# Kernel tuning notes

Measured on AMD Instinct MI355X. Metric: run time of the kernel, lower is better.

The kernel has to match this reference:

```python
import jax, jax.numpy as jnp
import numpy as np

B, T, IN, H0, H1, OUT = 128, 1024, 64, 256, 256, 64


def setup_inputs() -> dict:
    key = jax.random.key(0)
    ks = jax.random.split(key, 12)
    s0 = 1.0 / np.sqrt(H0)
    s1 = 1.0 / np.sqrt(H1)
    u = lambda k, shape, s: jax.random.uniform(k, shape, jnp.float32, -s, s)
    return {
        "input": jax.random.normal(ks[0], (B, T, IN), jnp.float32),
        # PyTorch LSTMCell params: weight_ih [4H, in], weight_hh [4H, H], biases [4H]
        "W_ih0": u(ks[1], (4 * H0, IN), s0),
        "W_hh0": u(ks[2], (4 * H0, H0), s0),
        "b_ih0": u(ks[3], (4 * H0,), s0),
        "b_hh0": u(ks[4], (4 * H0,), s0),
        "W_ih1": u(ks[5], (4 * H1, H0), s1),
        "W_hh1": u(ks[6], (4 * H1, H1), s1),
        "b_ih1": u(ks[7], (4 * H1,), s1),
        "b_hh1": u(ks[8], (4 * H1,), s1),
        "W_lin": u(ks[9], (OUT, H1), s1),
        "b_lin": u(ks[10], (OUT,), s1),
    }


def _lstm_cell(x_t, h, c, W_ih, W_hh, b):
    # gates in PyTorch order: i, f, g, o
    gates = x_t @ W_ih.T + h @ W_hh.T + b  # [B, 4H]
    i, f, g, o = jnp.split(gates, 4, axis=-1)
    c_new = jax.nn.sigmoid(f) * c + jax.nn.sigmoid(i) * jnp.tanh(g)
    h_new = jax.nn.sigmoid(o) * jnp.tanh(c_new)
    return h_new, c_new


def reference(input, W_ih0, W_hh0, b_ih0, b_hh0, W_ih1, W_hh1, b_ih1, b_hh1, W_lin, b_lin):
    b0 = b_ih0 + b_hh0
    b1 = b_ih1 + b_hh1
    batch = input.shape[0]
    h0 = jnp.zeros((batch, H0), input.dtype)
    c0 = jnp.zeros((batch, H0), input.dtype)
    h1 = jnp.zeros((batch, H1), input.dtype)
    c1 = jnp.zeros((batch, H1), input.dtype)

    def step(carry, x_t):
        h0, c0, h1, c1 = carry
        h0, c0 = _lstm_cell(x_t, h0, c0, W_ih0, W_hh0, b0)
        h1, c1 = _lstm_cell(h0, h1, c1, W_ih1, W_hh1, b1)
        out = h1 @ W_lin.T + b_lin  # [B, OUT]
        return (h0, c0, h1, c1), out

    xs = jnp.swapaxes(input, 0, 1)  # [T, B, IN]
    _, ys = jax.lax.scan(step, (h0, c0, h1, c1), xs)
    return jnp.swapaxes(ys, 0, 1)  # [B, T, OUT]
```

## Files before the change

kernel.cpp:

```cpp
#include <hip/hip_runtime.h>
#include <math.h>

#define TSEQ 1024
#define NB   128
#define NIN  64
#define NH   256
#define NOUT 64
#define NWG  256
#define NTHR 512
#define HS   (NH * NB)

__global__ void xpose_kernel(const float* __restrict__ in, float* __restrict__ xT) {
  __shared__ float tile[64 * 129];
  const int t = blockIdx.x;
  {
    const int b  = threadIdx.x >> 1;
    const int k0 = (threadIdx.x & 1) * 32;
    const float* src = in + (size_t)b * (TSEQ * NIN) + (size_t)t * NIN + k0;
#pragma unroll 8
    for (int k = 0; k < 32; ++k) tile[(k0 + k) * 129 + b] = src[k];
  }
  __syncthreads();
  {
    const int k  = threadIdx.x >> 2;
    const int b0 = (threadIdx.x & 3) * 32;
    float* dst = xT + (size_t)t * (NIN * NB) + (size_t)k * NB + b0;
#pragma unroll 8
    for (int i = 0; i < 32; ++i) dst[i] = tile[k * 129 + b0 + i];
  }
}

__device__ __forceinline__ float sigm(float v) { return 1.0f / (1.0f + expf(-v)); }

#define DPP_ADD(a, ctrl) do {                                                   \
  int _t = __builtin_amdgcn_update_dpp(0, __float_as_int(a), ctrl, 0xf, 0xf, true); \
  (a) += __int_as_float(_t); } while (0)

#define FMA32(w4, v0, v1) do {                                            \
  _Pragma("unroll")                                                        \
  for (int g = 0; g < 4; ++g) {                                            \
    float wg = (g == 0) ? (w4).x : (g == 1) ? (w4).y : (g == 2) ? (w4).z : (w4).w; \
    acc[g][0] += wg * (v0).x; acc[g][1] += wg * (v0).y;                    \
    acc[g][2] += wg * (v0).z; acc[g][3] += wg * (v0).w;                    \
    acc[g][4] += wg * (v1).x; acc[g][5] += wg * (v1).y;                    \
    acc[g][6] += wg * (v1).z; acc[g][7] += wg * (v1).w;                    \
  } } while (0)

__global__ __launch_bounds__(NTHR, 1) void lstm_persist(
    const float* __restrict__ x,
    const float* __restrict__ Wih0, const float* __restrict__ Whh0,
    const float* __restrict__ bih0, const float* __restrict__ bhh0,
    const float* __restrict__ Wih1, const float* __restrict__ Whh1,
    const float* __restrict__ bih1, const float* __restrict__ bhh1,
    const float* __restrict__ Wlin, const float* __restrict__ blin,
    float* __restrict__ out,
    float* __restrict__ h0T, float* __restrict__ h1T,
    const float* __restrict__ xT, unsigned* __restrict__ flags, int use_xT)
{
  __shared__ float Wt0[320 * 32];
  __shared__ float Wt1[512 * 32];
  __shared__ float Wlin2[2 * 256];
  __shared__ float red[8 * 580];
  __shared__ float redO[288];
  __shared__ float bias0[32], bias1[32], blinS[2];
  __shared__ float c0l[128], c1l[128];
  __shared__ float hs0[256 * 16];
  __shared__ float hs1[256 * 16];

  const int tid  = threadIdx.x;
  const int a    = blockIdx.x & 7;
  const int j    = blockIdx.x >> 3;
  const int b0   = a * 16;
  const int jh0  = j * 8;
  const int lane = tid & 63;
  const int wv   = tid >> 6;
  const int bh   = wv & 1;
  const int kw4  = wv >> 1;
  const int cl   = lane >> 3;
  const int kp   = lane & 7;
  const int kq   = kw4 * 8 + kp;

  for (int idx = tid; idx < 32 * 320; idx += NTHR) {
    int row = idx / 320, k = idx % 320;
    int c = row >> 2, g = row & 3;
    int grow = g * 256 + jh0 + c;
    float v = (k < 64) ? Wih0[grow * 64 + k] : Whh0[grow * 256 + (k - 64)];
    Wt0[k * 32 + row] = v;
  }
  for (int idx = tid; idx < 32 * 512; idx += NTHR) {
    int row = idx >> 9, k = idx & 511;
    int c = row >> 2, g = row & 3;
    int grow = g * 256 + jh0 + c;
    float v = (k < 256) ? Wih1[grow * 256 + k] : Whh1[grow * 256 + (k - 256)];
    Wt1[k * 32 + row] = v;
  }
  if (tid < 512) {
    int o2 = tid >> 8, k = tid & 255;
    Wlin2[tid] = Wlin[(2 * j + o2) * 256 + k];
  }
  if (tid < 32) {
    int c = tid >> 2, g = tid & 3;
    int grow = g * 256 + jh0 + c;
    bias0[tid] = bih0[grow] + bhh0[grow];
    bias1[tid] = bih1[grow] + bhh1[grow];
  }
  if (tid < 2) blinS[tid] = blin[2 * j + tid];
  if (tid < 128) { c0l[tid] = 0.0f; c1l[tid] = 0.0f; }
  __syncthreads();

  const int myflag = (a * 32 + j) * 16;

  for (int it = 0; it <= TSEQ + 1; ++it) {
    if (it >= 1 && tid < 64) {
      const unsigned tgt = (unsigned)it;
      const int fi = (a * 32 + (tid & 31)) * 16;
      while (true) {
        unsigned v = __hip_atomic_load(&flags[fi], __ATOMIC_RELAXED, __HIP_MEMORY_SCOPE_AGENT);
        if (__ballot(v >= tgt) == ~0ull) break;
        __builtin_amdgcn_s_sleep(1);
      }
    }
    __syncthreads();

    const float* h0r = h0T + ((it + 1) & 1) * HS;
    float*       h0w = h0T + (it & 1) * HS;
    const float* h1r = h1T + ((it + 1) % 3) * HS;
    float*       h1w = h1T + ((it + 2) % 3) * HS;

#pragma unroll
    for (int q = 0; q < 4; ++q) {
      int f = q * 512 + tid;
      int k = f >> 3, bi = f & 7;
      unsigned long long v0 = __hip_atomic_load(
          (const unsigned long long*)(h0r + (size_t)k * NB + b0) + bi,
          __ATOMIC_RELAXED, __HIP_MEMORY_SCOPE_AGENT);
      unsigned long long v1 = __hip_atomic_load(
          (const unsigned long long*)(h1r + (size_t)k * NB + b0) + bi,
          __ATOMIC_RELAXED, __HIP_MEMORY_SCOPE_AGENT);
      *(unsigned long long*)&hs0[f * 2] = v0;
      *(unsigned long long*)&hs1[f * 2] = v1;
    }
    __syncthreads();

    if (it < TSEQ) {
      float acc[4][8];
#pragma unroll
      for (int g = 0; g < 4; ++g)
#pragma unroll
        for (int b = 0; b < 8; ++b) acc[g][b] = 0.0f;
      if (use_xT) {
#pragma unroll
        for (int j2 = 0; j2 < 2; ++j2) {
          int k = j2 * 32 + kq;
          float4 w4 = *(const float4*)&Wt0[k * 32 + cl * 4];
          const float* xp = xT + (size_t)it * (NIN * NB) + (size_t)k * NB + b0 + bh * 8;
          float4 v0 = *(const float4*)xp;
          float4 v1 = *(const float4*)(xp + 4);
          FMA32(w4, v0, v1);
        }
      } else {
#pragma unroll
        for (int j2 = 0; j2 < 2; ++j2) {
          int k = j2 * 32 + kq;
          float4 w4 = *(const float4*)&Wt0[k * 32 + cl * 4];
          float xv[8];
#pragma unroll
          for (int b = 0; b < 8; ++b)
            xv[b] = x[(size_t)(b0 + bh * 8 + b) * (TSEQ * NIN) + (size_t)it * NIN + k];
          float4 v0 = make_float4(xv[0], xv[1], xv[2], xv[3]);
          float4 v1 = make_float4(xv[4], xv[5], xv[6], xv[7]);
          FMA32(w4, v0, v1);
        }
      }
#pragma unroll 4
      for (int j2 = 2; j2 < 10; ++j2) {
        int k = j2 * 32 + kq;
        float4 w4 = *(const float4*)&Wt0[k * 32 + cl * 4];
        const float* hp = &hs0[(k - 64) * 16 + bh * 8];
        float4 v0 = *(const float4*)hp;
        float4 v1 = *(const float4*)(hp + 4);
        FMA32(w4, v0, v1);
      }
#pragma unroll
      for (int g = 0; g < 4; ++g)
#pragma unroll
        for (int b = 0; b < 8; ++b) {
          DPP_ADD(acc[g][b], 0x104);
          DPP_ADD(acc[g][b], 0x102);
          DPP_ADD(acc[g][b], 0x101);
        }
      if (kp == 0) {
        int sbase = kw4 * 580 + (cl * 4) * 18 + bh * 8;
#pragma unroll
        for (int g = 0; g < 4; ++g)
#pragma unroll
          for (int b2 = 0; b2 < 4; ++b2)
            *(float2*)&red[sbase + g * 18 + 2 * b2] =
                make_float2(acc[g][2 * b2], acc[g][2 * b2 + 1]);
      }
    }
    if (it >= 1 && it <= TSEQ) {
      float acc[4][8];
#pragma unroll
      for (int g = 0; g < 4; ++g)
#pragma unroll
        for (int b = 0; b < 8; ++b) acc[g][b] = 0.0f;
#pragma unroll 4
      for (int j2 = 0; j2 < 8; ++j2) {
        int k = j2 * 32 + kq;
        float4 w4 = *(const float4*)&Wt1[k * 32 + cl * 4];
        const float* hp = &hs0[k * 16 + bh * 8];
        float4 v0 = *(const float4*)hp;
        float4 v1 = *(const float4*)(hp + 4);
        FMA32(w4, v0, v1);
      }
#pragma unroll 4
      for (int j2 = 8; j2 < 16; ++j2) {
        int k = j2 * 32 + kq;
        float4 w4 = *(const float4*)&Wt1[k * 32 + cl * 4];
        const float* hp = &hs1[(k - 256) * 16 + bh * 8];
        float4 v0 = *(const float4*)hp;
        float4 v1 = *(const float4*)(hp + 4);
        FMA32(w4, v0, v1);
      }
#pragma unroll
      for (int g = 0; g < 4; ++g)
#pragma unroll
        for (int b = 0; b < 8; ++b) {
          DPP_ADD(acc[g][b], 0x104);
          DPP_ADD(acc[g][b], 0x102);
          DPP_ADD(acc[g][b], 0x101);
        }
      if (kp == 0) {
        int sbase = (4 + kw4) * 580 + (cl * 4) * 18 + bh * 8;
#pragma unroll
        for (int g = 0; g < 4; ++g)
#pragma unroll
          for (int b2 = 0; b2 < 4; ++b2)
            *(float2*)&red[sbase + g * 18 + 2 * b2] =
                make_float2(acc[g][2 * b2], acc[g][2 * b2 + 1]);
      }
    }
    __syncthreads();

    if (tid < 128) {
      if (it < TSEQ) {
        int c = tid >> 4, b = tid & 15;
        float s0 = bias0[c * 4 + 0], s1 = bias0[c * 4 + 1];
        float s2 = bias0[c * 4 + 2], s3 = bias0[c * 4 + 3];
#pragma unroll
        for (int s = 0; s < 4; ++s) {
          int base = s * 580 + (c * 4) * 18 + b;
          s0 += red[base];      s1 += red[base + 18];
          s2 += red[base + 36]; s3 += red[base + 54];
        }
        float ig = sigm(s0), fg = sigm(s1), gg = tanhf(s2), og = sigm(s3);
        float cn = fg * c0l[tid] + ig * gg;
        c0l[tid] = cn;
        __hip_atomic_store(&h0w[(jh0 + c) * NB + b0 + b], og * tanhf(cn),
                           __ATOMIC_RELAXED, __HIP_MEMORY_SCOPE_AGENT);
      }
    } else if (tid < 256) {
      if (it >= 1 && it <= TSEQ) {
        int idx = tid - 128;
        int c = idx >> 4, b = idx & 15;
        float s0 = bias1[c * 4 + 0], s1 = bias1[c * 4 + 1];
        float s2 = bias1[c * 4 + 2], s3 = bias1[c * 4 + 3];
#pragma unroll
        for (int s = 4; s < 8; ++s) {
          int base = s * 580 + (c * 4) * 18 + b;
          s0 += red[base];      s1 += red[base + 18];
          s2 += red[base + 36]; s3 += red[base + 54];
        }
        float ig = sigm(s0), fg = sigm(s1), gg = tanhf(s2), og = sigm(s3);
        float cn = fg * c1l[idx] + ig * gg;
        c1l[idx] = cn;
        __hip_atomic_store(&h1w[(jh0 + c) * NB + b0 + b], og * tanhf(cn),
                           __ATOMIC_RELAXED, __HIP_MEMORY_SCOPE_AGENT);
      }
    } else {
      if (it >= 2) {
        int idx = tid & 255;
        int o2 = idx & 1, b = (idx >> 1) & 15, ks = idx >> 5;
        float acc = 0.0f;
#pragma unroll 8
        for (int k = 32 * ks; k < 32 * ks + 32; ++k)
          acc += Wlin2[o2 * 256 + k] * hs1[k * 16 + b];
        redO[(o2 * 16 + b) * 9 + ks] = acc;
      }
    }
    __syncthreads();

    if (it <= TSEQ && tid == 0) {
      asm volatile("" ::: "memory");
      __hip_atomic_store(&flags[myflag], (unsigned)(it + 1),
                         __ATOMIC_RELAXED, __HIP_MEMORY_SCOPE_AGENT);
    }

    if (it >= 2 && tid < 32) {
      int o2 = tid & 1, b = tid >> 1;
      float s = blinS[o2];
#pragma unroll
      for (int q = 0; q < 8; ++q) s += redO[(o2 * 16 + b) * 9 + q];
      out[(size_t)(b0 + b) * (TSEQ * NOUT) + (size_t)(it - 2) * NOUT + (2 * j + o2)] = s;
    }
  }
}

extern "C" void kernel_launch(void* const* d_in, const int* in_sizes, int n_in,
                              void* d_out, int out_size, void* d_ws, size_t ws_size,
                              hipStream_t stream) {
  const float* x    = (const float*)d_in[0];
  const float* Wih0 = (const float*)d_in[1];
  const float* Whh0 = (const float*)d_in[2];
  const float* bih0 = (const float*)d_in[3];
  const float* bhh0 = (const float*)d_in[4];
  const float* Wih1 = (const float*)d_in[5];
  const float* Whh1 = (const float*)d_in[6];
  const float* bih1 = (const float*)d_in[7];
  const float* bhh1 = (const float*)d_in[8];
  const float* Wlin = (const float*)d_in[9];
  const float* blin = (const float*)d_in[10];
  float* out = (float*)d_out;

  char* ws = (char*)d_ws;
  unsigned* flags = (unsigned*)ws;
  float* h0T = (float*)(ws + 16384);
  float* h1T = (float*)(ws + 16384 + 262144);
  float* xT  = (float*)(ws + (1 << 20));

  const size_t need_xT = (size_t)(1 << 20) + (size_t)TSEQ * NIN * NB * sizeof(float);
  const int use_xT = (ws_size >= need_xT) ? 1 : 0;

  size_t zbytes = (ws_size < (size_t)(1 << 20)) ? ws_size : (size_t)(1 << 20);
  hipMemsetAsync(d_ws, 0, zbytes, stream);

  if (use_xT) xpose_kernel<<<TSEQ, 256, 0, stream>>>(x, xT);

  lstm_persist<<<NWG, NTHR, 0, stream>>>(
      x, Wih0, Whh0, bih0, bhh0, Wih1, Whh1, bih1, bhh1, Wlin, blin,
      out, h0T, h1T, xT, flags, use_xT);
}
```

Baseline: 8.015 ms.

## Overlap x loads and output projection with flag wait; swizzle hidden staging

Moves the x-input load and the output-linear partial sums ahead of the inter-workgroup flag spin, so they overlap with the grid-wide wait. The output stage is delayed one more step and its computation is spread across all 512 threads. The layer-0 input FMAs now run between the global h loads and the shared-memory stores, hiding load latency. It also XOR-swizzles the hs0/hs1 layout to avoid LDS bank conflicts and keeps cell state in registers. In exchange the pipeline gets one extra iteration, an extra flag round, and more register pressure.

```diff
diff --git a/kernel.cpp b/kernel.cpp
--- a/kernel.cpp
+++ b/kernel.cpp
@@ -61,9 +61,8 @@
   __shared__ float Wt1[512 * 32];
   __shared__ float Wlin2[2 * 256];
   __shared__ float red[8 * 580];
-  __shared__ float redO[288];
+  __shared__ float redO[32 * 17];
   __shared__ float bias0[32], bias1[32], blinS[2];
-  __shared__ float c0l[128], c1l[128];
   __shared__ float hs0[256 * 16];
   __shared__ float hs1[256 * 16];
 
@@ -79,6 +78,12 @@
   const int cl   = lane >> 3;
   const int kp   = lane & 7;
   const int kq   = kw4 * 8 + kp;
+  const int bhx  = (bh ^ ((kp >> 1) & 1)) * 8;
+
+  const int oo2 = tid >> 8;
+  const int ob  = tid & 15;
+  const int oks = (tid & 255) >> 4;
+  const int obsw = ob ^ (((oks >> 1) & 1) * 8);
 
   for (int idx = tid; idx < 32 * 320; idx += NTHR) {
     int row = idx / 320, k = idx % 320;
@@ -105,13 +110,51 @@
     bias1[tid] = bih1[grow] + bhh1[grow];
   }
   if (tid < 2) blinS[tid] = blin[2 * j + tid];
-  if (tid < 128) { c0l[tid] = 0.0f; c1l[tid] = 0.0f; }
   __syncthreads();
 
   const int myflag = (a * 32 + j) * 16;
-
-  for (int it = 0; it <= TSEQ + 1; ++it) {
-    if (it >= 1 && tid < 64) {
+  float cstate = 0.0f;
+
+  for (int it = 0; it <= TSEQ + 2; ++it) {
+    const float* h0r = h0T + ((it + 1) & 1) * HS;
+    float*       h0w = h0T + (it & 1) * HS;
+    const float* h1r = h1T + ((it + 1) % 3) * HS;
+    float*       h1w = h1T + ((it + 2) % 3) * HS;
+
+    float4 xv[2][2];
+    if (it < TSEQ) {
+      if (use_xT) {
+#pragma unroll
+        for (int j2 = 0; j2 < 2; ++j2) {
+          int k = j2 * 32 + kq;
+          const float* xp = xT + (size_t)it * (NIN * NB) + (size_t)k * NB + b0 + bh * 8;
+          xv[j2][0] = *(const float4*)xp;
+          xv[j2][1] = *(const float4*)(xp + 4);
+        }
+      } else {
+#pragma unroll
+        for (int j2 = 0; j2 < 2; ++j2) {
+          int k = j2 * 32 + kq;
+          const float* xb = x + (size_t)(b0 + bh * 8) * (TSEQ * NIN) + (size_t)it * NIN + k;
+          float xs[8];
+#pragma unroll
+          for (int b = 0; b < 8; ++b) xs[b] = xb[(size_t)b * (TSEQ * NIN)];
+          xv[j2][0] = make_float4(xs[0], xs[1], xs[2], xs[3]);
+          xv[j2][1] = make_float4(xs[4], xs[5], xs[6], xs[7]);
+        }
+      }
+    }
+    if (it >= 3) {
+      float acc = 0.0f;
+#pragma unroll 4
+      for (int kk = 0; kk < 16; ++kk) {
+        int k = kk * 16 + oks;
+        acc += Wlin2[oo2 * 256 + k] * hs1[k * 16 + obsw];
+      }
+      redO[(oo2 * 16 + ob) * 17 + oks] = acc;
+    }
+
+    if (it >= 1 && it <= TSEQ + 1 && tid < 64) {
       const unsigned tgt = (unsigned)it;
       const int fi = (a * 32 + (tid & 31)) * 16;
       while (true) {
@@ -122,61 +165,55 @@
     }
     __syncthreads();
 
-    const float* h0r = h0T + ((it + 1) & 1) * HS;
-    float*       h0w = h0T + (it & 1) * HS;
-    const float* h1r = h1T + ((it + 1) % 3) * HS;
-    float*       h1w = h1T + ((it + 2) % 3) * HS;
-
-#pragma unroll
-    for (int q = 0; q < 4; ++q) {
-      int f = q * 512 + tid;
-      int k = f >> 3, bi = f & 7;
-      unsigned long long v0 = __hip_atomic_load(
-          (const unsigned long long*)(h0r + (size_t)k * NB + b0) + bi,
-          __ATOMIC_RELAXED, __HIP_MEMORY_SCOPE_AGENT);
-      unsigned long long v1 = __hip_atomic_load(
-          (const unsigned long long*)(h1r + (size_t)k * NB + b0) + bi,
-          __ATOMIC_RELAXED, __HIP_MEMORY_SCOPE_AGENT);
-      *(unsigned long long*)&hs0[f * 2] = v0;
-      *(unsigned long long*)&hs1[f * 2] = v1;
+    unsigned long long s0[4], s1[4];
+    const int stage_on = (it <= TSEQ + 1);
+    if (stage_on) {
+#pragma unroll
+      for (int q = 0; q < 4; ++q) {
+        int f = q * 512 + tid;
+        int k = f >> 3, bi = f & 7;
+        s0[q] = __hip_atomic_load(
+            (const unsigned long long*)(h0r + (size_t)k * NB + b0) + bi,
+            __ATOMIC_RELAXED, __HIP_MEMORY_SCOPE_AGENT);
+        s1[q] = __hip_atomic_load(
+            (const unsigned long long*)(h1r + (size_t)k * NB + b0) + bi,
+            __ATOMIC_RELAXED, __HIP_MEMORY_SCOPE_AGENT);
+      }
+    }
+
+    float accL0[4][8];
+#pragma unroll
+    for (int g = 0; g < 4; ++g)
+#pragma unroll
+      for (int b = 0; b < 8; ++b) accL0[g][b] = 0.0f;
+    if (it < TSEQ) {
+      float (*acc)[8] = accL0;
+#pragma unroll
+      for (int j2 = 0; j2 < 2; ++j2) {
+        float4 w4 = *(const float4*)&Wt0[(j2 * 32 + kq) * 32 + cl * 4];
+        FMA32(w4, xv[j2][0], xv[j2][1]);
+      }
+    }
+
+    if (stage_on) {
+#pragma unroll
+      for (int q = 0; q < 4; ++q) {
+        int f = q * 512 + tid;
+        int k = f >> 3, bi = f & 7;
+        int off = k * 16 + ((bi * 2) ^ (((k >> 1) & 1) * 8));
+        *(unsigned long long*)&hs0[off] = s0[q];
+        *(unsigned long long*)&hs1[off] = s1[q];
+      }
     }
     __syncthreads();
 
     if (it < TSEQ) {
-      float acc[4][8];
-#pragma unroll
-      for (int g = 0; g < 4; ++g)
-#pragma unroll
-        for (int b = 0; b < 8; ++b) acc[g][b] = 0.0f;
-      if (use_xT) {
-#pragma unroll
-        for (int j2 = 0; j2 < 2; ++j2) {
-          int k = j2 * 32 + kq;
-          float4 w4 = *(const float4*)&Wt0[k * 32 + cl * 4];
-          const float* xp = xT + (size_t)it * (NIN * NB) + (size_t)k * NB + b0 + bh * 8;
-          float4 v0 = *(const float4*)xp;
-          float4 v1 = *(const float4*)(xp + 4);
-          FMA32(w4, v0, v1);
-        }
-      } else {
-#pragma unroll
-        for (int j2 = 0; j2 < 2; ++j2) {
-          int k = j2 * 32 + kq;
-          float4 w4 = *(const float4*)&Wt0[k * 32 + cl * 4];
-          float xv[8];
-#pragma unroll
-          for (int b = 0; b < 8; ++b)
-            xv[b] = x[(size_t)(b0 + bh * 8 + b) * (TSEQ * NIN) + (size_t)it * NIN + k];
-          float4 v0 = make_float4(xv[0], xv[1], xv[2], xv[3]);
-          float4 v1 = make_float4(xv[4], xv[5], xv[6], xv[7]);
-          FMA32(w4, v0, v1);
-        }
-      }
+      float (*acc)[8] = accL0;
 #pragma unroll 4
-      for (int j2 = 2; j2 < 10; ++j2) {
-        int k = j2 * 32 + kq;
-        float4 w4 = *(const float4*)&Wt0[k * 32 + cl * 4];
-        const float* hp = &hs0[(k - 64) * 16 + bh * 8];
+      for (int j2 = 0; j2 < 8; ++j2) {
+        int kr = j2 * 32 + kq;
+        float4 w4 = *(const float4*)&Wt0[(64 + kr) * 32 + cl * 4];
+        const float* hp = &hs0[kr * 16 + bhx];
         float4 v0 = *(const float4*)hp;
         float4 v1 = *(const float4*)(hp + 4);
         FMA32(w4, v0, v1);
@@ -207,18 +244,18 @@
         for (int b = 0; b < 8; ++b) acc[g][b] = 0.0f;
 #pragma unroll 4
       for (int j2 = 0; j2 < 8; ++j2) {
-        int k = j2 * 32 + kq;
-        float4 w4 = *(const float4*)&Wt1[k * 32 + cl * 4];
-        const float* hp = &hs0[k * 16 + bh * 8];
+        int kr = j2 * 32 + kq;
+        float4 w4 = *(const float4*)&Wt1[kr * 32 + cl * 4];
+        const float* hp = &hs0[kr * 16 + bhx];
         float4 v0 = *(const float4*)hp;
         float4 v1 = *(const float4*)(hp + 4);
         FMA32(w4, v0, v1);
       }
 #pragma unroll 4
-      for (int j2 = 8; j2 < 16; ++j2) {
-        int k = j2 * 32 + kq;
-        float4 w4 = *(const float4*)&Wt1[k * 32 + cl * 4];
-        const float* hp = &hs1[(k - 256) * 16 + bh * 8];
+      for (int j2 = 0; j2 < 8; ++j2) {
+        int kr = j2 * 32 + kq;
+        float4 w4 = *(const float4*)&Wt1[(256 + kr) * 32 + cl * 4];
+        const float* hp = &hs1[kr * 16 + bhx];
         float4 v0 = *(const float4*)hp;
         float4 v1 = *(const float4*)(hp + 4);
         FMA32(w4, v0, v1);
@@ -255,8 +292,8 @@
           s2 += red[base + 36]; s3 += red[base + 54];
         }
         float ig = sigm(s0), fg = sigm(s1), gg = tanhf(s2), og = sigm(s3);
-        float cn = fg * c0l[tid] + ig * gg;
-        c0l[tid] = cn;
+        float cn = fg * cstate + ig * gg;
+        cstate = cn;
         __hip_atomic_store(&h0w[(jh0 + c) * NB + b0 + b], og * tanhf(cn),
                            __ATOMIC_RELAXED, __HIP_MEMORY_SCOPE_AGENT);
       }
@@ -273,36 +310,26 @@
           s2 += red[base + 36]; s3 += red[base + 54];
         }
         float ig = sigm(s0), fg = sigm(s1), gg = tanhf(s2), og = sigm(s3);
-        float cn = fg * c1l[idx] + ig * gg;
-        c1l[idx] = cn;
+        float cn = fg * cstate + ig * gg;
+        cstate = cn;
         __hip_atomic_store(&h1w[(jh0 + c) * NB + b0 + b], og * tanhf(cn),
                            __ATOMIC_RELAXED, __HIP_MEMORY_SCOPE_AGENT);
       }
-    } else {
-      if (it >= 2) {
-        int idx = tid & 255;
-        int o2 = idx & 1, b = (idx >> 1) & 15, ks = idx >> 5;
-        float acc = 0.0f;
-#pragma unroll 8
-        for (int k = 32 * ks; k < 32 * ks + 32; ++k)
-          acc += Wlin2[o2 * 256 + k] * hs1[k * 16 + b];
-        redO[(o2 * 16 + b) * 9 + ks] = acc;
+    } else if (tid < 288) {
+      if (it >= 3) {
+        int o2 = tid & 1, b = (tid >> 1) & 15;
+        float s = blinS[o2];
+#pragma unroll
+        for (int q = 0; q < 16; ++q) s += redO[(o2 * 16 + b) * 17 + q];
+        out[(size_t)(b0 + b) * (TSEQ * NOUT) + (size_t)(it - 3) * NOUT + (2 * j + o2)] = s;
       }
     }
     __syncthreads();
 
-    if (it <= TSEQ && tid == 0) {
+    if (it <= TSEQ + 1 && tid == 0) {
       asm volatile("" ::: "memory");
       __hip_atomic_store(&flags[myflag], (unsigned)(it + 1),
                          __ATOMIC_RELAXED, __HIP_MEMORY_SCOPE_AGENT);
-    }
-
-    if (it >= 2 && tid < 32) {
-      int o2 = tid & 1, b = tid >> 1;
-      float s = blinS[o2];
-#pragma unroll
-      for (int q = 0; q < 8; ++q) s += redO[(o2 * 16 + b) * 9 + q];
-      out[(size_t)(b0 + b) * (TSEQ * NOUT) + (size_t)(it - 2) * NOUT + (2 * j + o2)] = s;
     }
   }
 }
```

Result: faster. 6.665 ms (-16.8%).
